# Performance work log

Measured on AMD Instinct MI355X. Metric: run time of the kernel, lower is better.

Reference implementation:

```python
import jax, jax.numpy as jnp
import numpy as np

N = 50000      # nodes
E = 800000     # edges (avg degree 16)
IN = 128       # in_feats
OUT = 128      # out_feats
ASSIGN = 256   # assign_dim = B graphs * 8 clusters
B = 32         # batch_size (num graphs)


def setup_inputs() -> dict:
    key = jax.random.key(0)
    k0, k1, k2, k3 = jax.random.split(key, 4)
    x = jax.random.normal(k0, (N, IN), jnp.float32)
    edge_index = jax.random.randint(k1, (2, E), 0, N, dtype=jnp.int32)
    # sorted graph ids, ~equal-sized graphs (mirrors block_diag mask construction)
    batch = ((jnp.arange(N, dtype=jnp.int32) * B) // N).astype(jnp.int32)
    # SAGEConv params: Linear(2*in_feats -> out) on concat([x, mean_neigh])
    W_embed = jax.random.normal(k2, (2 * IN, OUT), jnp.float32) / np.float32(np.sqrt(2 * IN))
    b_embed = jnp.zeros((OUT,), jnp.float32)
    W_pool = jax.random.normal(k3, (2 * IN, ASSIGN), jnp.float32) / np.float32(np.sqrt(2 * IN))
    b_pool = jnp.zeros((ASSIGN,), jnp.float32)
    return dict(x=x, edge_index=edge_index, batch=batch,
                W_embed=W_embed, b_embed=b_embed, W_pool=W_pool, b_pool=b_pool)


def _sage(x, src, dst, W, b):
    # mean aggregation over in-neighbors (messages src -> dst), then Linear on concat
    n = x.shape[0]
    deg = jax.ops.segment_sum(jnp.ones((src.shape[0],), x.dtype), dst, num_segments=n)
    neigh = jax.ops.segment_sum(x[src], dst, num_segments=n) / jnp.maximum(deg, 1.0)[:, None]
    return jnp.concatenate([x, neigh], axis=-1) @ W + b


def reference(x, edge_index, batch, W_embed, b_embed, W_pool, b_pool):
    src, dst = edge_index[0], edge_index[1]
    embed = _sage(x, src, dst, W_embed, b_embed)                      # [N, OUT]
    pooled = jax.nn.softmax(_sage(x, src, dst, W_pool, b_pool), -1)   # [N, ASSIGN]
    # block-diagonal mask: node i of graph g sees columns [g*C, (g+1)*C)
    C = ASSIGN // B
    cols = jnp.arange(ASSIGN, dtype=batch.dtype) // C
    mask = (batch[:, None] == cols[None, :]).astype(x.dtype)          # [N, ASSIGN]
    # NOTE: faithful to original: softmax of (mask * pooled), zeros contribute exp(0)
    r = jax.nn.softmax(mask * pooled, axis=-1) * mask
    r = r / (r.sum(axis=-1, keepdims=True) + 1e-13)                   # [N, ASSIGN]
    h = r.T @ embed                                                   # [ASSIGN, OUT]
    # adj_new = S^T A S with A sparse COO (rows=edge_index[0], cols=edge_index[1])
    ar = jax.ops.segment_sum(r[dst], src, num_segments=x.shape[0])    # A @ S : [N, ASSIGN]
    adj_new = r.T @ ar                                                # [ASSIGN, ASSIGN]
    return (adj_new, h)
```

## Files before the change

### kernel.cpp

```cpp
#include <hip/hip_runtime.h>
#include <hip/hip_bf16.h>

#define N_ 50000
#define E_ 800000
#define IN_ 128
#define OUT_ 128
#define ASSIGN_ 256
#define B_ 32
#define KTOT 256
#define JTOT 384
#define HCHUNK 32
#define ACHUNK 32
#define AST 72
#define NXP ((N_ + 127) / 128)
#define NGB (NXP * 3)
#define NCVX 6250

#define NBKT 128
#define NPB 391
#define BCAP 7000
#define EPB 4096
#define NBLK_A ((E_ + EPB - 1) / EPB)
#define NPRE (NBLK_A + NCVX + 384)

typedef __attribute__((ext_vector_type(8))) short short8;
typedef __attribute__((ext_vector_type(4))) float f32x4;
typedef __attribute__((ext_vector_type(2))) float f32x2;
typedef __attribute__((ext_vector_type(4))) unsigned short ushort4v;
typedef __attribute__((ext_vector_type(2))) unsigned short ushort2v;
typedef unsigned short u16;

__device__ inline unsigned short f2bf(float v) {
    union { float f; unsigned u; } a;
    a.f = v;
    unsigned r = a.u + 0x7fff + ((a.u >> 16) & 1);
    return (unsigned short)(r >> 16);
}
__device__ inline float bf2f(unsigned short b) {
    union { unsigned u; float f; } a;
    a.u = ((unsigned)b) << 16;
    return a.f;
}

__device__ inline unsigned enc8(float v) {
    union { float f; unsigned u; } a;
    a.f = v * 0x1p-120f;
    unsigned b = a.u;
    unsigned r = b + 0x7FFFF + ((b >> 20) & 1);
    return ((r >> 20) & 0x7F) | ((b >> 24) & 0x80);
}
__device__ inline float2 dec8x2(unsigned short p) {
#if defined(__has_builtin) && __has_builtin(__builtin_amdgcn_cvt_pk_f32_fp8)
    f32x2 r = __builtin_amdgcn_cvt_pk_f32_fp8((int)(unsigned)p, false);
    return make_float2(r.x, r.y);
#else
    unsigned u0 = p & 0xffu, u1 = (p >> 8) & 0xffu;
    union { unsigned u; float f; } a, b;
    a.u = ((u0 & 0x80u) << 24) | ((u0 & 0x7fu) << 20);
    b.u = ((u1 & 0x80u) << 24) | ((u1 & 0x7fu) << 20);
    return make_float2(a.f * 0x1p+120f, b.f * 0x1p+120f);
#endif
}

__global__ __launch_bounds__(256) void k_pre(const int* __restrict__ ei,
                                             int* __restrict__ bktFill,
                                             int2* __restrict__ ebkt,
                                             const float* __restrict__ x,
                                             unsigned short* __restrict__ xhi,
                                             unsigned char* __restrict__ xq,
                                             const float* __restrict__ We,
                                             const float* __restrict__ be,
                                             const float* __restrict__ Wp,
                                             const float* __restrict__ bp,
                                             unsigned short* __restrict__ WThi,
                                             float* __restrict__ bias) {
    __shared__ int lh[NBKT], lbase[NBKT], lofs[NBKT];
    int bid = blockIdx.x;
    int t = threadIdx.x;
    if (bid < NBLK_A) {
        int e0 = bid * EPB;
        if (t < NBKT) { lh[t] = 0; lofs[t] = 0; }
        __syncthreads();
        int ss[16], dd[16];
#pragma unroll
        for (int i = 0; i < 16; i++) {
            int e = e0 + i * 256 + t;
            ss[i] = 0; dd[i] = -1;
            if (e < E_) {
                ss[i] = ei[e];
                dd[i] = ei[E_ + e];
                atomicAdd(&lh[dd[i] / NPB], 1);
            }
        }
        __syncthreads();
        if (t < NBKT) lbase[t] = t * BCAP + atomicAdd(&bktFill[t], lh[t]);
        __syncthreads();
#pragma unroll
        for (int i = 0; i < 16; i++) {
            if (dd[i] >= 0) {
                int b = dd[i] / NPB;
                int o = atomicAdd(&lofs[b], 1);
                ebkt[lbase[b] + o] = make_int2(ss[i], dd[i]);
            }
        }
        return;
    }
    if (bid >= NBLK_A + NCVX) {
        int idx = (bid - NBLK_A - NCVX) * 256 + t;
        if (idx < JTOT * KTOT) {
            int j = idx / KTOT, k = idx - j * KTOT;
            float v = (j < 128) ? We[k * 128 + j] : Wp[k * 256 + (j - 128)];
            WThi[idx] = f2bf(v);
        }
        if (idx < JTOT) bias[idx] = (idx < 128) ? be[idx] : bp[idx - 128];
        return;
    }
    int i4 = ((bid - NBLK_A) * 256 + t) * 4;
    if (i4 >= N_ * 128) return;
    float4 v = *(const float4*)(x + i4);
    ushort4v h;
    h.x = f2bf(v.x); h.y = f2bf(v.y); h.z = f2bf(v.z); h.w = f2bf(v.w);
    *(ushort4v*)(xhi + i4) = h;
    unsigned q = enc8(v.x) | (enc8(v.y) << 8) | (enc8(v.z) << 16) | (enc8(v.w) << 24);
    *(unsigned*)(xq + i4) = q;
}

__global__ __launch_bounds__(256) void k_binB(const int* __restrict__ bktFill,
                                              const int2* __restrict__ ebkt,
                                              int* __restrict__ ready,
                                              int* __restrict__ rowStart,
                                              int* __restrict__ csr_src,
                                              int* __restrict__ csr_dst) {
    __shared__ int ldeg[NPB];
    __shared__ int lscan[512];
    __shared__ int bsc[NBKT];
    __shared__ int lfill[NPB];
    int b = blockIdx.x, t = threadIdx.x;
    for (int i = t; i < NPB; i += 256) ldeg[i] = 0;
    __syncthreads();
    int base = b * BCAP;
    int cnt = bktFill[b];
    int n0 = b * NPB;
    for (int j = t; j < cnt; j += 256)
        atomicAdd(&ldeg[ebkt[base + j].y - n0], 1);
    __syncthreads();
    lscan[t] = (t < NPB) ? ldeg[t] : 0;
    lscan[t + 256] = (t + 256 < NPB) ? ldeg[t + 256] : 0;
    __syncthreads();
    for (int off = 1; off < 512; off <<= 1) {
        int x0 = lscan[t];
        int x1 = lscan[t + 256];
        int a0 = (t >= off) ? lscan[t - off] : 0;
        int a1 = (t + 256 >= off) ? lscan[t + 256 - off] : 0;
        __syncthreads();
        lscan[t] = x0 + a0;
        lscan[t + 256] = x1 + a1;
        __syncthreads();
    }
    if (t == 0) atomicExch(&ready[b], lscan[NPB - 1] + 1);
    if (t < NBKT) {
        int v;
        while ((v = atomicAdd(&ready[t], 0)) == 0) __builtin_amdgcn_s_sleep(8);
        bsc[t] = v - 1;
    }
    __syncthreads();
    for (int off = 1; off < NBKT; off <<= 1) {
        int x = (t < NBKT) ? bsc[t] : 0;
        int add = (t < NBKT && t >= off) ? bsc[t - off] : 0;
        __syncthreads();
        if (t < NBKT) bsc[t] = x + add;
        __syncthreads();
    }
    int base0 = (b == 0) ? 0 : bsc[b - 1];
    for (int i = t; i < NPB; i += 256) {
        int n = n0 + i;
        if (n < N_) {
            int excl = (i == 0) ? 0 : lscan[i - 1];
            lfill[i] = excl;
            rowStart[n] = base0 + excl;
        }
    }
    __syncthreads();
    for (int j = t; j < cnt; j += 256) {
        int2 sd = ebkt[base + j];
        int p = base0 + atomicAdd(&lfill[sd.y - n0], 1);
        csr_src[p] = sd.x;
        csr_dst[p] = sd.y;
    }
    if (b == 0 && t == 0) rowStart[N_] = E_;
}

__global__ __launch_bounds__(256) void k_agg(const unsigned char* __restrict__ xq,
                                             const int* __restrict__ rowStart,
                                             const int* __restrict__ csr_src,
                                             unsigned short* __restrict__ nhi) {
    int node = blockIdx.x * 4 + (threadIdx.x >> 6);
    if (node >= N_) return;
    int lane = threadIdx.x & 63;
    int l5 = lane & 31;
    int eh = lane >> 5;
    int a = rowStart[node], bnd = rowStart[node + 1];
    float a0 = 0.f, a1 = 0.f, a2 = 0.f, a3 = 0.f;
    int j = a;
    for (; j + 7 < bnd; j += 8) {
        unsigned q[4];
#pragma unroll
        for (int ii = 0; ii < 4; ii++) {
            int s = csr_src[j + 2 * ii + eh];
            q[ii] = *(const unsigned*)(xq + (size_t)s * 128 + l5 * 4);
        }
#pragma unroll
        for (int ii = 0; ii < 4; ii++) {
            float2 f01 = dec8x2((unsigned short)(q[ii] & 0xffffu));
            float2 f23 = dec8x2((unsigned short)(q[ii] >> 16));
            a0 += f01.x; a1 += f01.y; a2 += f23.x; a3 += f23.y;
        }
    }
    for (; j < bnd; j += 2) {
        unsigned qq = 0;
        int e = j + eh;
        if (e < bnd) {
            int s = csr_src[e];
            qq = *(const unsigned*)(xq + (size_t)s * 128 + l5 * 4);
        }
        float2 f01 = dec8x2((unsigned short)(qq & 0xffffu));
        float2 f23 = dec8x2((unsigned short)(qq >> 16));
        a0 += f01.x; a1 += f01.y; a2 += f23.x; a3 += f23.y;
    }
    a0 += __shfl_xor(a0, 32, 64);
    a1 += __shfl_xor(a1, 32, 64);
    a2 += __shfl_xor(a2, 32, 64);
    a3 += __shfl_xor(a3, 32, 64);
    float inv = 1.0f / (float)max(bnd - a, 1);
    if (lane < 32) {
        ushort4v h;
        h.x = f2bf(a0 * inv);
        h.y = f2bf(a1 * inv);
        h.z = f2bf(a2 * inv);
        h.w = f2bf(a3 * inv);
        *(ushort4v*)(nhi + (size_t)node * 128 + l5 * 4) = h;
    }
}

#define LDA 40
__global__ __launch_bounds__(256) void k_gemm(const unsigned short* __restrict__ xhi,
                                              const unsigned short* __restrict__ nhi,
                                              const unsigned short* __restrict__ WThi,
                                              const float* __restrict__ bias,
                                              unsigned short* __restrict__ embed,
                                              unsigned short* __restrict__ plog) {
    __shared__ __align__(16) union {
        struct { u16 Ah[128][LDA]; u16 Bh[128][LDA]; } s;
        u16 ep[64 * 128];
    } sm;
    int t = threadIdx.x;
    int wave = t >> 6, lane = t & 63;
    int wm = wave >> 1, wn = wave & 1;
    int q = lane >> 4, lr = lane & 15;

    int id = blockIdx.x;
    int xi, cc;
    if (id < (NXP / 8) * 24) {
        xi = (id / 24) * 8 + (id & 7);
        cc = (id % 24) >> 3;
    } else {
        int r2 = id - (NXP / 8) * 24;
        xi = (NXP / 8) * 8 + r2 % (NXP % 8);
        cc = r2 / (NXP % 8);
    }
    int row0 = xi * 128;
    int col0 = cc * 128;

    f32x4 acc[4][4] = {};
    int smr = t >> 1;
    int kc = (t & 1) * 16;
    int node = row0 + smr;

    short8 vh0, vh1, wh0, wh1;
#define LOADK(KT)                                                                    \
    {                                                                                \
        const u16* Ah_src = ((KT) < 128) ? xhi : nhi;                                \
        int kb = ((KT) & 127) + kc;                                                  \
        vh0 = {}; vh1 = {};                                                          \
        if (node < N_) {                                                             \
            const short8* ph = (const short8*)(Ah_src + (size_t)node * 128 + kb);    \
            vh0 = ph[0]; vh1 = ph[1];                                                \
        }                                                                            \
        const short8* pw = (const short8*)(WThi + (size_t)(col0 + smr) * 256 + (KT) + kc); \
        wh0 = pw[0]; wh1 = pw[1];                                                    \
    }
    LOADK(0);
    for (int kt = 0; kt < KTOT; kt += 32) {
        *(short8*)&sm.s.Ah[smr][kc] = vh0;
        *(short8*)&sm.s.Ah[smr][kc + 8] = vh1;
        *(short8*)&sm.s.Bh[smr][kc] = wh0;
        *(short8*)&sm.s.Bh[smr][kc + 8] = wh1;
        __syncthreads();
        if (kt + 32 < KTOT) LOADK(kt + 32);

        short8 afh[4];
#pragma unroll
        for (int mi = 0; mi < 4; mi++) {
            int r = wm * 64 + mi * 16 + lr;
            afh[mi] = *(const short8*)&sm.s.Ah[r][q * 8];
        }
#pragma unroll
        for (int ni = 0; ni < 4; ni++) {
            int r = wn * 64 + ni * 16 + lr;
            short8 bfh = *(const short8*)&sm.s.Bh[r][q * 8];
#pragma unroll
            for (int mi = 0; mi < 4; mi++)
                acc[mi][ni] = __builtin_amdgcn_mfma_f32_16x16x32_bf16(afh[mi], bfh, acc[mi][ni], 0, 0, 0);
        }
        __syncthreads();
    }
#undef LOADK

    for (int half = 0; half < 2; half++) {
        __syncthreads();
        if (wm == half) {
#pragma unroll
            for (int mi = 0; mi < 4; mi++)
#pragma unroll
                for (int ni = 0; ni < 4; ni++) {
                    int lcol = wn * 64 + ni * 16 + lr;
                    float bj = bias[col0 + lcol];
#pragma unroll
                    for (int r = 0; r < 4; r++) {
                        int lrow = mi * 16 + q * 4 + r;
                        sm.ep[lrow * 128 + lcol] = f2bf(acc[mi][ni][r] + bj);
                    }
                }
        }
        __syncthreads();
#pragma unroll
        for (int i = 0; i < 4; i++) {
            int chunk = i * 256 + t;
            int lrow = chunk >> 4;
            int lco = (chunk & 15) * 8;
            int grow = row0 + half * 64 + lrow;
            if (grow < N_) {
                short8 v = *(const short8*)&sm.ep[lrow * 128 + lco];
                if (col0 < 128)
                    *(short8*)(embed + (size_t)grow * 128 + lco) = v;
                else
                    *(short8*)(plog + (size_t)grow * 256 + (col0 - 128) + lco) = v;
            }
        }
    }
}

__global__ __launch_bounds__(256) void k_r(const unsigned short* __restrict__ plog,
                                           const int* __restrict__ batch,
                                           float* __restrict__ r8,
                                           unsigned short* __restrict__ r8b) {
    int node = blockIdx.x * 4 + (threadIdx.x >> 6);
    int lane = threadIdx.x & 63;
    if (node >= N_) return;
    ushort4v p4 = *(const ushort4v*)(plog + (size_t)node * 256 + lane * 4);
    float px = bf2f(p4.x), py = bf2f(p4.y), pz = bf2f(p4.z), pw = bf2f(p4.w);
    float m = fmaxf(fmaxf(px, py), fmaxf(pz, pw));
    for (int off = 32; off; off >>= 1) m = fmaxf(m, __shfl_xor(m, off, 64));
    float s = expf(px - m) + expf(py - m) + expf(pz - m) + expf(pw - m);
    for (int off = 32; off; off >>= 1) s += __shfl_xor(s, off, 64);
    int g = batch[node];
    float v = 0.f;
    if (lane < 8) v = expf(bf2f(plog[(size_t)node * 256 + g * 8 + lane]) - m) / s;
    float M2 = v;
    for (int off = 4; off; off >>= 1) M2 = fmaxf(M2, __shfl_xor(M2, off, 64));
    float e = expf(v - M2);
    float Sg = e;
    for (int off = 4; off; off >>= 1) Sg += __shfl_xor(Sg, off, 64);
    float D2 = Sg + 248.0f * expf(-M2);
    float r = e / (Sg + 1e-13f * D2);
    if (lane < 8) {
        r8[node * 8 + lane] = r;
        r8b[node * 8 + lane] = f2bf(r);
    }
}

__global__ __launch_bounds__(256) void k_tail(const int* __restrict__ rowStart,
                                              const int* __restrict__ csr_src,
                                              const int* __restrict__ csr_dst,
                                              const unsigned short* __restrict__ r8b,
                                              float* __restrict__ partAdj,
                                              const unsigned short* __restrict__ embed,
                                              const float* __restrict__ r8,
                                              float* __restrict__ partH) {
    __shared__ __align__(16) unsigned short Ab[256 * AST];
    __shared__ __align__(16) unsigned short Bb[16 * AST];
    int id = blockIdx.x;
    int t = threadIdx.x;
    if (id >= B_ * ACHUNK) {
        int idh = id - B_ * ACHUNK;
        int g = idh & 31;
        int c = idh >> 5;
        int o = t & 127, half = t >> 7;
        int n0g = (g * N_ + 31) >> 5;
        int n1g = ((g + 1) * N_ + 31) >> 5;
        int len = n1g - n0g;
        int a = n0g + (len * c) / HCHUNK;
        int b = n0g + (len * (c + 1)) / HCHUNK;
        float a0 = 0.f, a1 = 0.f, a2 = 0.f, a3 = 0.f;
#pragma unroll 4
        for (int n = a; n < b; n++) {
            float e = bf2f(embed[(size_t)n * 128 + o]);
            const float* rr = r8 + n * 8 + half;
            a0 += rr[0] * e;
            a1 += rr[2] * e;
            a2 += rr[4] * e;
            a3 += rr[6] * e;
        }
        float* pb = partH + (g * HCHUNK + c) * 1024;
        pb[(half + 0) * 128 + o] = a0;
        pb[(half + 2) * 128 + o] = a1;
        pb[(half + 4) * 128 + o] = a2;
        pb[(half + 6) * 128 + o] = a3;
        return;
    }
    int gd = id & 31;
    int c = id >> 5;
    int wave = t >> 6, lane = t & 63;
    int q = lane >> 4, lr = lane & 15;
    int n0g = (gd * N_ + 31) >> 5;
    int n1g = ((gd + 1) * N_ + 31) >> 5;
    int len = n1g - n0g;
    int na = n0g + (len * c) / ACHUNK;
    int nb = n0g + (len * (c + 1)) / ACHUNK;
    int j0 = rowStart[na], j1 = rowStart[nb];

    uint4 z = {0, 0, 0, 0};
#pragma unroll
    for (int i = 0; i < 9; i++) *(uint4*)&Ab[(i * 256 + t) * 8] = z;
    if (t < 144) *(uint4*)&Bb[t * 8] = z;
    __syncthreads();

    f32x4 acc[4] = {};
    int el = t >> 2;
    int ap = t & 3;

    for (int jt = j0; jt < j1; jt += 64) {
        int j = jt + el;
        int ca = -1;
        if (j < j1) {
            int s = csr_src[j];
            int d = csr_dst[j];
            int gs = (s * B_) / N_;
            unsigned sv = *(const unsigned*)(r8b + (size_t)s * 8 + ap * 2);
            unsigned dv = *(const unsigned*)(r8b + (size_t)d * 8 + ap * 2);
            ca = gs * 8 + ap * 2;
            Ab[ca * AST + el] = (unsigned short)sv;
            Ab[(ca + 1) * AST + el] = (unsigned short)(sv >> 16);
            Bb[(ap * 2) * AST + el] = (unsigned short)dv;
            Bb[(ap * 2 + 1) * AST + el] = (unsigned short)(dv >> 16);
        }
        __syncthreads();
        short8 bf0 = *(const short8*)&Bb[lr * AST + q * 8];
        short8 bf1 = *(const short8*)&Bb[lr * AST + 32 + q * 8];
#pragma unroll
        for (int mi = 0; mi < 4; mi++) {
            int col = (wave * 4 + mi) * 16 + lr;
            short8 a0 = *(const short8*)&Ab[col * AST + q * 8];
            short8 a1 = *(const short8*)&Ab[col * AST + 32 + q * 8];
            acc[mi] = __builtin_amdgcn_mfma_f32_16x16x32_bf16(a0, bf0, acc[mi], 0, 0, 0);
            acc[mi] = __builtin_amdgcn_mfma_f32_16x16x32_bf16(a1, bf1, acc[mi], 0, 0, 0);
        }
        __syncthreads();
        if (ca >= 0) {
            Ab[ca * AST + el] = 0;
            Ab[(ca + 1) * AST + el] = 0;
            Bb[(ap * 2) * AST + el] = 0;
            Bb[(ap * 2 + 1) * AST + el] = 0;
        }
        __syncthreads();
    }

    float* pb = partAdj + (gd * ACHUNK + c) * 2048;
    if (lr < 8) {
#pragma unroll
        for (int mi = 0; mi < 4; mi++) {
            int mbase = (wave * 4 + mi) * 16 + q * 4;
#pragma unroll
            for (int r = 0; r < 4; r++)
                pb[(mbase + r) * 8 + lr] = acc[mi][r];
        }
    }
}

__global__ __launch_bounds__(256) void k_red(const float* __restrict__ partAdj,
                                             const float* __restrict__ partH,
                                             float* __restrict__ out) {
    int o = blockIdx.x * 256 + threadIdx.x;
    if (o < 256 * 256) {
        int row = o >> 8, col = o & 255;
        int gd = col >> 3, b = col & 7;
        int li = row * 8 + b;
        float s = 0.f;
#pragma unroll
        for (int c = 0; c < ACHUNK; c++) s += partAdj[(gd * ACHUNK + c) * 2048 + li];
        out[o] = s;
    } else {
        int idx = o - 256 * 256;
        int g = idx >> 10;
        int local = idx & 1023;
        float s = 0.f;
#pragma unroll
        for (int c = 0; c < HCHUNK; c++) s += partH[(g * HCHUNK + c) * 1024 + local];
        out[256 * 256 + idx] = s;
    }
}

extern "C" void kernel_launch(void* const* d_in, const int* in_sizes, int n_in,
                              void* d_out, int out_size, void* d_ws, size_t ws_size,
                              hipStream_t stream) {
    const float* x = (const float*)d_in[0];
    const int* ei = (const int*)d_in[1];
    const int* batch = (const int*)d_in[2];
    const float* We = (const float*)d_in[3];
    const float* be = (const float*)d_in[4];
    const float* Wp = (const float*)d_in[5];
    const float* bp = (const float*)d_in[6];
    float* out = (float*)d_out;

    char* w = (char*)d_ws;
    auto alloc = [&](size_t bytes) -> char* {
        char* p = w;
        w += (bytes + 255) & ~(size_t)255;
        return p;
    };
    unsigned short* xhi = (unsigned short*)alloc((size_t)N_ * 128 * 2);
    unsigned char* xq = (unsigned char*)alloc((size_t)N_ * 128);
    unsigned short* nhi = (unsigned short*)alloc((size_t)N_ * 128 * 2);
    unsigned short* WThi = (unsigned short*)alloc((size_t)JTOT * KTOT * 2);
    unsigned short* embed = (unsigned short*)alloc((size_t)N_ * 128 * 2);
    unsigned short* plog = (unsigned short*)alloc((size_t)N_ * 256 * 2);
    float* r8 = (float*)alloc((size_t)N_ * 8 * 4);
    unsigned short* r8b = (unsigned short*)alloc((size_t)N_ * 8 * 2);
    float* bias = (float*)alloc(JTOT * 4);
    int* rowStart = (int*)alloc((size_t)(N_ + 1) * 4);
    int* csr_src = (int*)alloc((size_t)E_ * 4);
    int* csr_dst = (int*)alloc((size_t)E_ * 4);
    int* bktFill = (int*)alloc(2 * NBKT * 4);
    int* ready = bktFill + NBKT;
    int2* ebkt = (int2*)alloc((size_t)NBKT * BCAP * 8);
    float* partH = (float*)alloc((size_t)B_ * HCHUNK * 1024 * 4);
    float* partAdj = (float*)alloc((size_t)B_ * ACHUNK * 2048 * 4);

    hipMemsetAsync(bktFill, 0, 2 * NBKT * 4, stream);
    k_pre<<<NPRE, 256, 0, stream>>>(ei, bktFill, ebkt, x, xhi, xq, We, be, Wp, bp, WThi, bias);
    k_binB<<<NBKT, 256, 0, stream>>>(bktFill, ebkt, ready, rowStart, csr_src, csr_dst);
    k_agg<<<(N_ + 3) / 4, 256, 0, stream>>>(xq, rowStart, csr_src, nhi);
    k_gemm<<<NGB, 256, 0, stream>>>(xhi, nhi, WThi, bias, embed, plog);
    k_r<<<(N_ + 3) / 4, 256, 0, stream>>>(plog, batch, r8, r8b);
    k_tail<<<2 * B_ * ACHUNK, 256, 0, stream>>>(rowStart, csr_src, csr_dst, r8b, partAdj, embed, r8, partH);
    k_red<<<(256 * 256 + 256 * 128 + 255) / 256, 256, 0, stream>>>(partAdj, partH, out);
}
```

Measured before the change: 224.2 us.

## Widen neighbor gather to 16-byte loads and fuse final reduction into tail kernel

The aggregation kernel now has each group of 8 lanes cover one edge with 16-byte loads of the fp8 row. That gives 8 edges per wave step instead of 2, with a 3-stage shuffle reduction at the end. The separate reduction kernel is removed: each tail block increments a per-graph counter, and the last block to finish sums the partials and writes the output. This cuts one kernel launch and raises memory-level parallelism in the gather, at the cost of more registers (16 accumulators) and a serialized last-block reduction.

```diff
diff --git a/kernel.cpp b/kernel.cpp
--- a/kernel.cpp
+++ b/kernel.cpp
@@ -197,48 +197,62 @@
     int node = blockIdx.x * 4 + (threadIdx.x >> 6);
     if (node >= N_) return;
     int lane = threadIdx.x & 63;
-    int l5 = lane & 31;
-    int eh = lane >> 5;
+    int es = lane >> 3;
+    int fb = lane & 7;
     int a = rowStart[node], bnd = rowStart[node + 1];
-    float a0 = 0.f, a1 = 0.f, a2 = 0.f, a3 = 0.f;
+    float acc[16];
+#pragma unroll
+    for (int k = 0; k < 16; k++) acc[k] = 0.f;
+#define DEC(Q)                                                       \
+    {                                                                \
+        unsigned wq[4] = {(Q).x, (Q).y, (Q).z, (Q).w};               \
+        _Pragma("unroll")                                            \
+        for (int wi = 0; wi < 4; wi++) {                             \
+            float2 f01 = dec8x2((unsigned short)(wq[wi] & 0xffffu)); \
+            float2 f23 = dec8x2((unsigned short)(wq[wi] >> 16));     \
+            acc[wi * 4 + 0] += f01.x; acc[wi * 4 + 1] += f01.y;      \
+            acc[wi * 4 + 2] += f23.x; acc[wi * 4 + 3] += f23.y;      \
+        }                                                            \
+    }
     int j = a;
-    for (; j + 7 < bnd; j += 8) {
-        unsigned q[4];
-#pragma unroll
-        for (int ii = 0; ii < 4; ii++) {
-            int s = csr_src[j + 2 * ii + eh];
-            q[ii] = *(const unsigned*)(xq + (size_t)s * 128 + l5 * 4);
-        }
-#pragma unroll
-        for (int ii = 0; ii < 4; ii++) {
-            float2 f01 = dec8x2((unsigned short)(q[ii] & 0xffffu));
-            float2 f23 = dec8x2((unsigned short)(q[ii] >> 16));
-            a0 += f01.x; a1 += f01.y; a2 += f23.x; a3 += f23.y;
-        }
-    }
-    for (; j < bnd; j += 2) {
-        unsigned qq = 0;
-        int e = j + eh;
-        if (e < bnd) {
-            int s = csr_src[e];
-            qq = *(const unsigned*)(xq + (size_t)s * 128 + l5 * 4);
-        }
-        float2 f01 = dec8x2((unsigned short)(qq & 0xffffu));
-        float2 f23 = dec8x2((unsigned short)(qq >> 16));
-        a0 += f01.x; a1 += f01.y; a2 += f23.x; a3 += f23.y;
-    }
-    a0 += __shfl_xor(a0, 32, 64);
-    a1 += __shfl_xor(a1, 32, 64);
-    a2 += __shfl_xor(a2, 32, 64);
-    a3 += __shfl_xor(a3, 32, 64);
+    for (; j + 8 < bnd; j += 16) {
+        int s0 = csr_src[j + es];
+        uint4 q0 = *(const uint4*)(xq + (size_t)s0 * 128 + fb * 16);
+        uint4 q1 = {0, 0, 0, 0};
+        int e1 = j + 8 + es;
+        if (e1 < bnd) {
+            int s1 = csr_src[e1];
+            q1 = *(const uint4*)(xq + (size_t)s1 * 128 + fb * 16);
+        }
+        DEC(q0);
+        DEC(q1);
+    }
+    if (j < bnd) {
+        uint4 q0 = {0, 0, 0, 0};
+        int e0 = j + es;
+        if (e0 < bnd) {
+            int s0 = csr_src[e0];
+            q0 = *(const uint4*)(xq + (size_t)s0 * 128 + fb * 16);
+        }
+        DEC(q0);
+    }
+#undef DEC
+#pragma unroll
+    for (int k = 0; k < 16; k++) {
+        acc[k] += __shfl_xor(acc[k], 8, 64);
+        acc[k] += __shfl_xor(acc[k], 16, 64);
+        acc[k] += __shfl_xor(acc[k], 32, 64);
+    }
     float inv = 1.0f / (float)max(bnd - a, 1);
-    if (lane < 32) {
-        ushort4v h;
-        h.x = f2bf(a0 * inv);
-        h.y = f2bf(a1 * inv);
-        h.z = f2bf(a2 * inv);
-        h.w = f2bf(a3 * inv);
-        *(ushort4v*)(nhi + (size_t)node * 128 + l5 * 4) = h;
+    if (es == 0) {
+        short8 o0, o1;
+#pragma unroll
+        for (int k = 0; k < 8; k++) {
+            o0[k] = (short)f2bf(acc[k] * inv);
+            o1[k] = (short)f2bf(acc[k + 8] * inv);
+        }
+        *(short8*)(nhi + (size_t)node * 128 + fb * 16) = o0;
+        *(short8*)(nhi + (size_t)node * 128 + fb * 16 + 8) = o1;
     }
 }
 
@@ -386,9 +400,13 @@
                                               float* __restrict__ partAdj,
                                               const unsigned short* __restrict__ embed,
                                               const float* __restrict__ r8,
-                                              float* __restrict__ partH) {
+                                              float* __restrict__ partH,
+                                              int* __restrict__ adjCnt,
+                                              int* __restrict__ hCnt,
+                                              float* __restrict__ out) {
     __shared__ __align__(16) unsigned short Ab[256 * AST];
     __shared__ __align__(16) unsigned short Bb[16 * AST];
+    __shared__ int lastFlag;
     int id = blockIdx.x;
     int t = threadIdx.x;
     if (id >= B_ * ACHUNK) {
@@ -416,6 +434,19 @@
         pb[(half + 2) * 128 + o] = a1;
         pb[(half + 4) * 128 + o] = a2;
         pb[(half + 6) * 128 + o] = a3;
+        __threadfence();
+        __syncthreads();
+        if (t == 0) lastFlag = (atomicAdd(&hCnt[g], 1) == HCHUNK - 1) ? 1 : 0;
+        __syncthreads();
+        if (lastFlag) {
+            __threadfence();
+            for (int oo = t; oo < 1024; oo += 256) {
+                float s = 0.f;
+#pragma unroll
+                for (int c2 = 0; c2 < HCHUNK; c2++) s += partH[(g * HCHUNK + c2) * 1024 + oo];
+                out[256 * 256 + g * 1024 + oo] = s;
+            }
+        }
         return;
     }
     int gd = id & 31;
@@ -485,28 +516,20 @@
                 pb[(mbase + r) * 8 + lr] = acc[mi][r];
         }
     }
-}
-
-__global__ __launch_bounds__(256) void k_red(const float* __restrict__ partAdj,
-                                             const float* __restrict__ partH,
-                                             float* __restrict__ out) {
-    int o = blockIdx.x * 256 + threadIdx.x;
-    if (o < 256 * 256) {
-        int row = o >> 8, col = o & 255;
-        int gd = col >> 3, b = col & 7;
-        int li = row * 8 + b;
-        float s = 0.f;
-#pragma unroll
-        for (int c = 0; c < ACHUNK; c++) s += partAdj[(gd * ACHUNK + c) * 2048 + li];
-        out[o] = s;
-    } else {
-        int idx = o - 256 * 256;
-        int g = idx >> 10;
-        int local = idx & 1023;
-        float s = 0.f;
-#pragma unroll
-        for (int c = 0; c < HCHUNK; c++) s += partH[(g * HCHUNK + c) * 1024 + local];
-        out[256 * 256 + idx] = s;
+    __threadfence();
+    __syncthreads();
+    if (t == 0) lastFlag = (atomicAdd(&adjCnt[gd], 1) == ACHUNK - 1) ? 1 : 0;
+    __syncthreads();
+    if (lastFlag) {
+        __threadfence();
+        for (int oo = t; oo < 2048; oo += 256) {
+            int row = oo >> 3, bb = oo & 7;
+            int li = row * 8 + bb;
+            float s = 0.f;
+#pragma unroll
+            for (int c2 = 0; c2 < ACHUNK; c2++) s += partAdj[(gd * ACHUNK + c2) * 2048 + li];
+            out[row * 256 + gd * 8 + bb] = s;
+        }
     }
 }
 
@@ -540,18 +563,21 @@
     int* rowStart = (int*)alloc((size_t)(N_ + 1) * 4);
     int* csr_src = (int*)alloc((size_t)E_ * 4);
     int* csr_dst = (int*)alloc((size_t)E_ * 4);
-    int* bktFill = (int*)alloc(2 * NBKT * 4);
-    int* ready = bktFill + NBKT;
+    int* flags = (int*)alloc((2 * NBKT + 64) * 4);
+    int* bktFill = flags;
+    int* ready = flags + NBKT;
+    int* adjCnt = flags + 2 * NBKT;
+    int* hCnt = flags + 2 * NBKT + 32;
     int2* ebkt = (int2*)alloc((size_t)NBKT * BCAP * 8);
     float* partH = (float*)alloc((size_t)B_ * HCHUNK * 1024 * 4);
     float* partAdj = (float*)alloc((size_t)B_ * ACHUNK * 2048 * 4);
 
-    hipMemsetAsync(bktFill, 0, 2 * NBKT * 4, stream);
+    hipMemsetAsync(flags, 0, (2 * NBKT + 64) * 4, stream);
     k_pre<<<NPRE, 256, 0, stream>>>(ei, bktFill, ebkt, x, xhi, xq, We, be, Wp, bp, WThi, bias);
     k_binB<<<NBKT, 256, 0, stream>>>(bktFill, ebkt, ready, rowStart, csr_src, csr_dst);
     k_agg<<<(N_ + 3) / 4, 256, 0, stream>>>(xq, rowStart, csr_src, nhi);
     k_gemm<<<NGB, 256, 0, stream>>>(xhi, nhi, WThi, bias, embed, plog);
     k_r<<<(N_ + 3) / 4, 256, 0, stream>>>(plog, batch, r8, r8b);
-    k_tail<<<2 * B_ * ACHUNK, 256, 0, stream>>>(rowStart, csr_src, csr_dst, r8b, partAdj, embed, r8, partH);
-    k_red<<<(256 * 256 + 256 * 128 + 255) / 256, 256, 0, stream>>>(partAdj, partH, out);
-}
+    k_tail<<<2 * B_ * ACHUNK, 256, 0, stream>>>(rowStart, csr_src, csr_dst, r8b, partAdj,
+                                                embed, r8, partH, adjCnt, hCnt, out);
+}
```

Result: slower. 434.3 us (+93.7%).
